# Performance work log

Measured on AMD Instinct MI355X. Metric: run time of the kernel, lower is better.

## Reference

```python
import jax, jax.numpy as jnp
import numpy as np

N_INTT = 100000
N_MVTX = 100000
N_EDGES = 300000
IN_DIM = 64
OUT_DIM = 64
FEAT_DIM = 2 * OUT_DIM          # 128
EDGE_DIM = 2 * FEAT_DIM         # 256
H_DIM = IN_DIM + FEAT_DIM + 2 * EDGE_DIM  # 64+128+512 = 704


def _lin(key, fan_in, fan_out):
    k1, k2 = jax.random.split(key)
    bound = 1.0 / np.sqrt(fan_in)
    W = jax.random.uniform(k1, (fan_in, fan_out), jnp.float32, -bound, bound)
    b = jax.random.uniform(k2, (fan_out,), jnp.float32, -bound, bound)
    return W, b


def setup_inputs() -> dict:
    key = jax.random.key(0)
    ks = jax.random.split(key, 12)
    x_intt_0 = jax.random.normal(ks[0], (N_INTT, 3), jnp.float32)
    x_mvtx_0 = jax.random.normal(ks[1], (N_MVTX, 3), jnp.float32)
    x_intt = jax.random.normal(ks[2], (N_INTT, IN_DIM), jnp.float32)
    x_mvtx = jax.random.normal(ks[3], (N_MVTX, IN_DIM), jnp.float32)
    start = jax.random.randint(ks[4], (N_EDGES,), 0, N_INTT, jnp.int32)
    end = jax.random.randint(ks[5], (N_EDGES,), 0, N_MVTX, jnp.int32)
    edge_index = jnp.stack([start, end], axis=0)
    W_in_intt, b_in_intt = _lin(ks[6], IN_DIM, FEAT_DIM)
    W_in_mvtx, b_in_mvtx = _lin(ks[7], IN_DIM, FEAT_DIM)
    W_score, b_score = _lin(ks[8], EDGE_DIM, 1)
    W_out_intt, b_out_intt = _lin(ks[9], H_DIM, OUT_DIM)
    W_out_mvtx, b_out_mvtx = _lin(ks[10], H_DIM, OUT_DIM)
    return {
        "x_intt_0": x_intt_0, "x_mvtx_0": x_mvtx_0,
        "x_intt": x_intt, "x_mvtx": x_mvtx, "edge_index": edge_index,
        "W_in_intt": W_in_intt, "b_in_intt": b_in_intt,
        "W_in_mvtx": W_in_mvtx, "b_in_mvtx": b_in_mvtx,
        "W_score": W_score, "b_score": b_score,
        "W_out_intt": W_out_intt, "b_out_intt": b_out_intt,
        "W_out_mvtx": W_out_mvtx, "b_out_mvtx": b_out_mvtx,
    }


def _mean_max_pool(edges, idx, num_segments):
    # scatter_mean with zero-initialized out: mean over incident edges, 0 if none
    s = jax.ops.segment_sum(edges, idx, num_segments=num_segments)
    cnt = jax.ops.segment_sum(jnp.ones((edges.shape[0], 1), edges.dtype), idx,
                              num_segments=num_segments)
    mean = s / jnp.maximum(cnt, 1.0)
    # scatter_max with zero-initialized out: max includes the initial 0
    mx = jnp.maximum(jax.ops.segment_max(edges, idx, num_segments=num_segments), 0.0)
    return mean, mx


def reference(x_intt_0, x_mvtx_0, x_intt, x_mvtx, edge_index,
              W_in_intt, b_in_intt, W_in_mvtx, b_in_mvtx,
              W_score, b_score, W_out_intt, b_out_intt,
              W_out_mvtx, b_out_mvtx):
    # apply_constraints=False -> x_intt_0/x_mvtx_0 unused
    xp_intt = x_intt @ W_in_intt + b_in_intt        # [Ni, F]
    xp_mvtx = x_mvtx @ W_in_mvtx + b_in_mvtx        # [Nm, F]
    start, end = edge_index[0], edge_index[1]
    xp = jnp.concatenate([xp_intt[start], xp_mvtx[end]], axis=-1)  # [E, 2F]
    att = jnp.exp(-jnp.abs(xp @ W_score + b_score))  # potential activation, [E,1]
    edges = xp * att                                 # [E, 2F]
    mean_i, max_i = _mean_max_pool(edges, start, xp_intt.shape[0])
    mean_m, max_m = _mean_max_pool(edges, end, xp_mvtx.shape[0])
    H_intt = jnp.concatenate([x_intt, xp_intt, mean_i, max_i], axis=-1)  # [Ni, 704]
    H_mvtx = jnp.concatenate([x_mvtx, xp_mvtx, mean_m, max_m], axis=-1)
    h_intt = jax.nn.relu(H_intt @ W_out_intt + b_out_intt)
    h_mvtx = jax.nn.relu(H_mvtx @ W_out_mvtx + b_out_mvtx)
    return (h_intt, h_mvtx)
```

## Files before the change

kernel.cpp:

```cpp
#include <hip/hip_runtime.h>
#include <hip/hip_bf16.h>

typedef __hip_bfloat16 bf16;
typedef __attribute__((ext_vector_type(8))) short bf16x8;
typedef __attribute__((ext_vector_type(4))) float f32x4;

__device__ __forceinline__ float bfu(unsigned u) { return __uint_as_float(u << 16); }
__device__ __forceinline__ unsigned packbf(float a, float b) {
    return (unsigned)__bfloat16_as_ushort(__float2bfloat16(a)) |
           ((unsigned)__bfloat16_as_ushort(__float2bfloat16(b)) << 16);
}

#define CAP 32

#define NEL_O (704 * 64)

__global__ __launch_bounds__(256) void prep_kernel(
    const int* __restrict__ e_start, const int* __restrict__ e_end,
    int* __restrict__ deg_i, int* __restrict__ deg_m,
    int* __restrict__ list_i, int* __restrict__ list_m, int E, int fill_blocks,
    const float* __restrict__ Woi, const float* __restrict__ Wom,
    bf16* __restrict__ Wtoi, bf16* __restrict__ Wtom,
    const float* __restrict__ Wii, const float* __restrict__ Wim, int wt_blocks,
    const float* __restrict__ x_i, const float* __restrict__ b_i,
    const float* __restrict__ x_m, const float* __restrict__ b_m,
    const float* __restrict__ Wsc,
    bf16* __restrict__ xp_i, bf16* __restrict__ xp_m,
    float* __restrict__ sc_i, float* __restrict__ sc_m,
    int Ni, int Nm, int lin_bi)
{
    int bid = blockIdx.x;
    if (bid < fill_blocks) {
        int i = bid * 256 + threadIdx.x;
        if (i >= E) return;
        int s = e_start[i], e = e_end[i];
        int pi = atomicAdd(&deg_i[s], 1);
        if (pi < CAP) list_i[(size_t)s * CAP + pi] = e;
        int pm = atomicAdd(&deg_m[e], 1);
        if (pm < CAP) list_m[(size_t)e * CAP + pm] = s;
        return;
    }
    bid -= fill_blocks;
    if (bid < wt_blocks) {
        int tid = bid * 256 + threadIdx.x;
        if (tid >= 2 * NEL_O) return;
        int half = tid >= NEL_O;
        int t = tid - half * NEL_O;
        int j = t / 704, k = t % 704;
        const float* W = half ? Wom : Woi;
        bf16* Wt = half ? Wtom : Wtoi;
        Wt[(size_t)j * 704 + k] = __float2bfloat16(W[(size_t)k * 64 + j]);
        return;
    }
    bid -= wt_blocks;
    int side = bid >= lin_bi;
    int blk = side ? bid - lin_bi : bid;
    const float* x   = side ? x_m : x_i;
    const float* Win = side ? Wim : Wii;
    const float* b   = side ? b_m : b_i;
    const float* wsc = side ? Wsc + 128 : Wsc;
    bf16* xp = side ? xp_m : xp_i;
    float* sc = side ? sc_m : sc_i;
    int N = side ? Nm : Ni;

    int tid = threadIdx.x, wv = tid >> 6, lane = tid & 63;
    int frow = lane & 15, kg = lane >> 4;
    int n0 = blk * 64 + wv * 16;
    if (n0 >= N) return;
    int nrow = min(n0 + frow, N - 1);
    f32x4 acc[8];
#pragma unroll
    for (int nt = 0; nt < 8; ++nt) acc[nt] = (f32x4){0.f, 0.f, 0.f, 0.f};
#pragma unroll
    for (int kk = 0; kk < 2; ++kk) {
        const float* ap = x + (size_t)nrow * 64 + kk * 32 + kg * 8;
        float4 a0 = *(const float4*)ap;
        float4 a1 = *(const float4*)(ap + 4);
        union { unsigned u[4]; bf16x8 v; } au;
        au.u[0] = packbf(a0.x, a0.y); au.u[1] = packbf(a0.z, a0.w);
        au.u[2] = packbf(a1.x, a1.y); au.u[3] = packbf(a1.z, a1.w);
#pragma unroll
        for (int nt = 0; nt < 8; ++nt) {
            int col = nt * 16 + frow;
            const float* wp = Win + (size_t)(kk * 32 + kg * 8) * 128 + col;
            union { unsigned u[4]; bf16x8 v; } bu;
#pragma unroll
            for (int z = 0; z < 4; ++z)
                bu.u[z] = packbf(wp[(2 * z) * 128], wp[(2 * z + 1) * 128]);
            acc[nt] = __builtin_amdgcn_mfma_f32_16x16x32_bf16(au.v, bu.v, acc[nt], 0, 0, 0);
        }
    }
    float contrib[4] = {0.f, 0.f, 0.f, 0.f};
#pragma unroll
    for (int nt = 0; nt < 8; ++nt) {
        int col = nt * 16 + frow;
        float bj = b[col];
        float wj = wsc[col];
#pragma unroll
        for (int reg = 0; reg < 4; ++reg) {
            float v = acc[nt][reg] + bj;
            int n = n0 + kg * 4 + reg;
            if (n < N) xp[(size_t)n * 128 + col] = __float2bfloat16(v);
            contrib[reg] += v * wj;
        }
    }
#pragma unroll
    for (int off = 1; off < 16; off <<= 1) {
#pragma unroll
        for (int reg = 0; reg < 4; ++reg)
            contrib[reg] += __shfl_xor(contrib[reg], off, 64);
    }
    if (frow == 0) {
#pragma unroll
        for (int reg = 0; reg < 4; ++reg) {
            int n = n0 + kg * 4 + reg;
            if (n < N) sc[n] = contrib[reg];
        }
    }
}

#define BN 16
#define HS 716
__device__ __forceinline__ void accum8(uint4 g, float att, float* s, float* m) {
    unsigned gg[4] = {g.x, g.y, g.z, g.w};
#pragma unroll
    for (int k = 0; k < 4; ++k) {
        float t0 = att * bfu(gg[k] & 0xffffu);
        float t1 = att * bfu(gg[k] >> 16);
        s[2 * k] += t0;  s[2 * k + 1] += t1;
        m[2 * k] = fmaxf(m[2 * k], t0);  m[2 * k + 1] = fmaxf(m[2 * k + 1], t1);
    }
}

__global__ __launch_bounds__(256) void node_kernel(
    const float* __restrict__ x_i, const bf16* __restrict__ xp_i,
    const bf16* __restrict__ xp_m,
    const float* __restrict__ sc_i, const float* __restrict__ sc_m,
    const int* __restrict__ deg_i, const int* __restrict__ list_i,
    const bf16* __restrict__ Wt_oi, const float* __restrict__ b_oi,
    const float* __restrict__ x_m,
    const int* __restrict__ deg_m, const int* __restrict__ list_m,
    const bf16* __restrict__ Wt_om, const float* __restrict__ b_om,
    const float* __restrict__ bsc, float* __restrict__ out,
    int Ni, int Nm, int blocks_i)
{
    __shared__ bf16 Hs[BN][HS];
    int side = (int)blockIdx.x >= blocks_i;
    int blk = side ? blockIdx.x - blocks_i : blockIdx.x;
    const float* x        = side ? x_m : x_i;
    const bf16* xp_self   = side ? xp_m : xp_i;
    const bf16* xp_other  = side ? xp_i : xp_m;
    const float* sc_self  = side ? sc_m : sc_i;
    const float* sc_other = side ? sc_i : sc_m;
    const int* deg  = side ? deg_m : deg_i;
    const int* list = side ? list_m : list_i;
    const bf16* Wt  = side ? Wt_om : Wt_oi;
    const float* b  = side ? b_om : b_oi;
    float* outp = side ? out + (size_t)Ni * 64 : out;
    int N = side ? Nm : Ni;
    int self_first = side ? 0 : 1;

    int tid = threadIdx.x, wv = tid >> 6, lane = tid & 63;
    int ql = lane & 15, q4 = lane & 48;
    int r = wv * 4 + (lane >> 4);
    int n0 = blk * BN;
    int n = min(n0 + r, N - 1);

    float bias = bsc[0];
    int dg = deg[n];
    int dgc = min(dg, CAP);
    float ps = sc_self[n] + bias;
    uint4 us4 = *(const uint4*)(xp_self + (size_t)n * 128 + ql * 8);
    float4 xv4 = *(const float4*)(x + (size_t)n * 64 + ql * 4);

    int oa = 0, ob = 0;
    float sa = 0.f, sb = 0.f;
    if (ql < dgc)      oa = list[(size_t)n * CAP + ql];
    if (16 + ql < dgc) ob = list[(size_t)n * CAP + 16 + ql];
    if (ql < dgc)      sa = sc_other[oa];
    if (16 + ql < dgc) sb = sc_other[ob];
    float att_a = (ql < dgc)      ? __expf(-fabsf(ps + sa)) : 0.f;
    float att_b = (16 + ql < dgc) ? __expf(-fabsf(ps + sb)) : 0.f;

    float A = att_a + att_b;
    float Am = fmaxf(att_a, att_b);
#pragma unroll
    for (int off = 1; off < 16; off <<= 1) {
        A += __shfl_xor(A, off, 64);
        Am = fmaxf(Am, __shfl_xor(Am, off, 64));
    }

    float s[8], m[8];
#pragma unroll
    for (int k = 0; k < 8; ++k) { s[k] = 0.f; m[k] = 0.f; }

    int dmaxw = dgc;
    dmaxw = max(dmaxw, __shfl_xor(dmaxw, 16, 64));
    dmaxw = max(dmaxw, __shfl_xor(dmaxw, 32, 64));

    int dm0 = min(dmaxw, 16);
    for (int d = 0; d < dm0; d += 4) {
        uint4 g[4];
        float a[4];
#pragma unroll
        for (int j = 0; j < 4; ++j) {
            int dd = min(d + j, 15);
            bool p = (d + j < dgc);
            int o = __shfl(oa, q4 + dd, 64);
            a[j] = p ? __shfl(att_a, q4 + dd, 64) : 0.f;
            g[j] = (uint4){0u, 0u, 0u, 0u};
            if (p) g[j] = *(const uint4*)(xp_other + (size_t)o * 128 + ql * 8);
        }
#pragma unroll
        for (int j = 0; j < 4; ++j) accum8(g[j], a[j], s, m);
    }
    for (int d = 16; d < dmaxw; d += 2) {
#pragma unroll
        for (int j = 0; j < 2; ++j) {
            int dd = min(d + j - 16, 15);
            bool p = (d + j < dgc);
            int o = __shfl(ob, q4 + dd, 64);
            float a0 = p ? __shfl(att_b, q4 + dd, 64) : 0.f;
            uint4 g0 = (uint4){0u, 0u, 0u, 0u};
            if (p) g0 = *(const uint4*)(xp_other + (size_t)o * 128 + ql * 8);
            accum8(g0, a0, s, m);
        }
    }

    float inv = 1.0f / fmaxf((float)dg, 1.0f);
    float sA = A * inv, sAm = Am;
    int cm_self  = self_first ? 192 : 320;
    int cm_cross = self_first ? 320 : 192;
    int cx_self  = self_first ? 448 : 576;
    int cx_cross = self_first ? 576 : 448;
    char* row = (char*)&Hs[r][0];
    *(uint2*)(row + ql * 8) = make_uint2(packbf(xv4.x, xv4.y), packbf(xv4.z, xv4.w));
    *(uint4*)(row + 128 + ql * 16) = us4;
    unsigned uu[4] = {us4.x, us4.y, us4.z, us4.w};
    float xs[8];
#pragma unroll
    for (int k = 0; k < 4; ++k) {
        xs[2 * k] = bfu(uu[k] & 0xffffu);
        xs[2 * k + 1] = bfu(uu[k] >> 16);
    }
    uint4 wms, wxs, wmc, wxc;
    wms.x = packbf(xs[0] * sA, xs[1] * sA);  wms.y = packbf(xs[2] * sA, xs[3] * sA);
    wms.z = packbf(xs[4] * sA, xs[5] * sA);  wms.w = packbf(xs[6] * sA, xs[7] * sA);
    wxs.x = packbf(fmaxf(xs[0], 0.f) * sAm, fmaxf(xs[1], 0.f) * sAm);
    wxs.y = packbf(fmaxf(xs[2], 0.f) * sAm, fmaxf(xs[3], 0.f) * sAm);
    wxs.z = packbf(fmaxf(xs[4], 0.f) * sAm, fmaxf(xs[5], 0.f) * sAm);
    wxs.w = packbf(fmaxf(xs[6], 0.f) * sAm, fmaxf(xs[7], 0.f) * sAm);
    wmc.x = packbf(s[0] * inv, s[1] * inv);  wmc.y = packbf(s[2] * inv, s[3] * inv);
    wmc.z = packbf(s[4] * inv, s[5] * inv);  wmc.w = packbf(s[6] * inv, s[7] * inv);
    wxc.x = packbf(m[0], m[1]);  wxc.y = packbf(m[2], m[3]);
    wxc.z = packbf(m[4], m[5]);  wxc.w = packbf(m[6], m[7]);
    *(uint4*)(row + cm_self * 2 + ql * 16)  = wms;
    *(uint4*)(row + cx_self * 2 + ql * 16)  = wxs;
    *(uint4*)(row + cm_cross * 2 + ql * 16) = wmc;
    *(uint4*)(row + cx_cross * 2 + ql * 16) = wxc;
    __syncthreads();

    int frow = lane & 15;
    int kg = lane >> 4;
    const char* abase = (const char*)&Hs[frow][0] + kg * 16;
    const char* bbase = (const char*)(Wt + (size_t)(wv * 16 + frow) * 704) + kg * 16;
    f32x4 acc = {0.f, 0.f, 0.f, 0.f};
#pragma unroll
    for (int kt = 0; kt < 22; ++kt) {
        bf16x8 a  = *(const bf16x8*)(abase + kt * 64);
        bf16x8 bf = *(const bf16x8*)(bbase + kt * 64);
        acc = __builtin_amdgcn_mfma_f32_16x16x32_bf16(a, bf, acc, 0, 0, 0);
    }
    int ccol = wv * 16 + frow;
    float bj = b[ccol];
#pragma unroll
    for (int reg = 0; reg < 4; ++reg) {
        int crow = kg * 4 + reg;
        int nn = n0 + crow;
        if (nn < N) outp[(size_t)nn * 64 + ccol] = fmaxf(acc[reg] + bj, 0.f);
    }
}

extern "C" void kernel_launch(void* const* d_in, const int* in_sizes, int n_in,
                              void* d_out, int out_size, void* d_ws, size_t ws_size,
                              hipStream_t stream) {
    const float* x_i    = (const float*)d_in[2];
    const float* x_m    = (const float*)d_in[3];
    const int*   eidx   = (const int*)d_in[4];
    const float* W_in_i = (const float*)d_in[5];
    const float* b_in_i = (const float*)d_in[6];
    const float* W_in_m = (const float*)d_in[7];
    const float* b_in_m = (const float*)d_in[8];
    const float* W_sc   = (const float*)d_in[9];
    const float* b_sc   = (const float*)d_in[10];
    const float* W_o_i  = (const float*)d_in[11];
    const float* b_o_i  = (const float*)d_in[12];
    const float* W_o_m  = (const float*)d_in[13];
    const float* b_o_m  = (const float*)d_in[14];

    int Ni = in_sizes[2] / 64;
    int Nm = in_sizes[3] / 64;
    int E  = in_sizes[4] / 2;
    const int* e_start = eidx;
    const int* e_end   = eidx + E;

    char* base = (char*)d_ws;
    bf16* xp_i  = (bf16*)base;  base += (size_t)Ni * 128 * sizeof(bf16);
    bf16* xp_m  = (bf16*)base;  base += (size_t)Nm * 128 * sizeof(bf16);
    float* sc_i = (float*)base; base += (size_t)Ni * sizeof(float);
    float* sc_m = (float*)base; base += (size_t)Nm * sizeof(float);
    int* list_i = (int*)base;   base += (size_t)Ni * CAP * sizeof(int);
    int* list_m = (int*)base;   base += (size_t)Nm * CAP * sizeof(int);
    int* deg_i  = (int*)base;   base += (size_t)Ni * sizeof(int);
    int* deg_m  = (int*)base;   base += (size_t)Nm * sizeof(int);
    bf16* Wt_oi = (bf16*)base;  base += (size_t)704 * 64 * sizeof(bf16);
    bf16* Wt_om = (bf16*)base;  base += (size_t)704 * 64 * sizeof(bf16);
    hipMemsetAsync(deg_i, 0, ((size_t)Ni + Nm) * sizeof(int), stream);

    int fill_blocks = (E + 255) / 256;
    int wt_blocks = (2 * NEL_O + 255) / 256;
    int lin_bi = (Ni + 63) / 64, lin_bm = (Nm + 63) / 64;
    prep_kernel<<<fill_blocks + wt_blocks + lin_bi + lin_bm, 256, 0, stream>>>(
        e_start, e_end, deg_i, deg_m, list_i, list_m, E, fill_blocks,
        W_o_i, W_o_m, Wt_oi, Wt_om, W_in_i, W_in_m, wt_blocks,
        x_i, b_in_i, x_m, b_in_m, W_sc,
        xp_i, xp_m, sc_i, sc_m, Ni, Nm, lin_bi);

    float* out = (float*)d_out;
    int nb_i = (Ni + BN - 1) / BN, nb_m = (Nm + BN - 1) / BN;
    node_kernel<<<nb_i + nb_m, 256, 0, stream>>>(
        x_i, xp_i, xp_m, sc_i, sc_m, deg_i, list_i, Wt_oi, b_o_i,
        x_m, deg_m, list_m, Wt_om, b_o_m, b_sc, out, Ni, Nm, nb_i);
}
```

Before: 221.7 us.

## Assign one wavefront per node in node kernel gather with 1024-thread blocks

Node aggregation now gives each node a full 64-lane wavefront that gathers 4-byte slices of each neighbor row, instead of 16 lanes per node gathering 16-byte slices. Blocks grow to 1024 threads (16 waves, one per node), and only the first four waves run the MFMA output projection. The aim is more memory-level parallelism and more uniform per-wave loop trip counts. In exchange, loads become narrower, there are more shuffles per edge, and 12 of 16 waves sit idle during the matmul phase. The large blocks with launch bounds of (1024, 8) may also limit occupancy or register allocation.

```diff
diff --git a/kernel.cpp b/kernel.cpp
--- a/kernel.cpp
+++ b/kernel.cpp
@@ -121,18 +121,7 @@
 
 #define BN 16
 #define HS 716
-__device__ __forceinline__ void accum8(uint4 g, float att, float* s, float* m) {
-    unsigned gg[4] = {g.x, g.y, g.z, g.w};
-#pragma unroll
-    for (int k = 0; k < 4; ++k) {
-        float t0 = att * bfu(gg[k] & 0xffffu);
-        float t1 = att * bfu(gg[k] >> 16);
-        s[2 * k] += t0;  s[2 * k + 1] += t1;
-        m[2 * k] = fmaxf(m[2 * k], t0);  m[2 * k + 1] = fmaxf(m[2 * k + 1], t1);
-    }
-}
-
-__global__ __launch_bounds__(256) void node_kernel(
+__global__ __launch_bounds__(1024, 8) void node_kernel(
     const float* __restrict__ x_i, const bf16* __restrict__ xp_i,
     const bf16* __restrict__ xp_m,
     const float* __restrict__ sc_i, const float* __restrict__ sc_m,
@@ -161,69 +150,46 @@
     int self_first = side ? 0 : 1;
 
     int tid = threadIdx.x, wv = tid >> 6, lane = tid & 63;
-    int ql = lane & 15, q4 = lane & 48;
-    int r = wv * 4 + (lane >> 4);
     int n0 = blk * BN;
-    int n = min(n0 + r, N - 1);
+    int n = min(n0 + wv, N - 1);
 
     float bias = bsc[0];
     int dg = deg[n];
     int dgc = min(dg, CAP);
     float ps = sc_self[n] + bias;
-    uint4 us4 = *(const uint4*)(xp_self + (size_t)n * 128 + ql * 8);
-    float4 xv4 = *(const float4*)(x + (size_t)n * 64 + ql * 4);
-
-    int oa = 0, ob = 0;
-    float sa = 0.f, sb = 0.f;
-    if (ql < dgc)      oa = list[(size_t)n * CAP + ql];
-    if (16 + ql < dgc) ob = list[(size_t)n * CAP + 16 + ql];
-    if (ql < dgc)      sa = sc_other[oa];
-    if (16 + ql < dgc) sb = sc_other[ob];
-    float att_a = (ql < dgc)      ? __expf(-fabsf(ps + sa)) : 0.f;
-    float att_b = (16 + ql < dgc) ? __expf(-fabsf(ps + sb)) : 0.f;
-
-    float A = att_a + att_b;
-    float Am = fmaxf(att_a, att_b);
-#pragma unroll
-    for (int off = 1; off < 16; off <<= 1) {
+    unsigned us = *(const unsigned*)(xp_self + (size_t)n * 128 + 2 * lane);
+    float xv = x[(size_t)n * 64 + lane];
+
+    int o = (lane < 32) ? list[(size_t)n * CAP + lane] : 0;
+    float sco = (lane < dgc) ? sc_other[o] : 0.f;
+    float att = (lane < dgc) ? __expf(-fabsf(ps + sco)) : 0.f;
+
+    float A = att, Am = att;
+#pragma unroll
+    for (int off = 1; off < 64; off <<= 1) {
         A += __shfl_xor(A, off, 64);
         Am = fmaxf(Am, __shfl_xor(Am, off, 64));
     }
 
-    float s[8], m[8];
-#pragma unroll
-    for (int k = 0; k < 8; ++k) { s[k] = 0.f; m[k] = 0.f; }
-
-    int dmaxw = dgc;
-    dmaxw = max(dmaxw, __shfl_xor(dmaxw, 16, 64));
-    dmaxw = max(dmaxw, __shfl_xor(dmaxw, 32, 64));
-
-    int dm0 = min(dmaxw, 16);
-    for (int d = 0; d < dm0; d += 4) {
-        uint4 g[4];
+    float s0 = 0.f, s1 = 0.f, m0 = 0.f, m1 = 0.f;
+    for (int d = 0; d < dgc; d += 4) {
+        unsigned g[4];
         float a[4];
 #pragma unroll
         for (int j = 0; j < 4; ++j) {
-            int dd = min(d + j, 15);
+            int dd = min(d + j, CAP - 1);
             bool p = (d + j < dgc);
-            int o = __shfl(oa, q4 + dd, 64);
-            a[j] = p ? __shfl(att_a, q4 + dd, 64) : 0.f;
-            g[j] = (uint4){0u, 0u, 0u, 0u};
-            if (p) g[j] = *(const uint4*)(xp_other + (size_t)o * 128 + ql * 8);
-        }
-#pragma unroll
-        for (int j = 0; j < 4; ++j) accum8(g[j], a[j], s, m);
-    }
-    for (int d = 16; d < dmaxw; d += 2) {
-#pragma unroll
-        for (int j = 0; j < 2; ++j) {
-            int dd = min(d + j - 16, 15);
-            bool p = (d + j < dgc);
-            int o = __shfl(ob, q4 + dd, 64);
-            float a0 = p ? __shfl(att_b, q4 + dd, 64) : 0.f;
-            uint4 g0 = (uint4){0u, 0u, 0u, 0u};
-            if (p) g0 = *(const uint4*)(xp_other + (size_t)o * 128 + ql * 8);
-            accum8(g0, a0, s, m);
+            int oo = __shfl(o, dd, 64);
+            a[j] = p ? __shfl(att, dd, 64) : 0.f;
+            g[j] = 0u;
+            if (p) g[j] = *(const unsigned*)(xp_other + (size_t)oo * 128 + 2 * lane);
+        }
+#pragma unroll
+        for (int j = 0; j < 4; ++j) {
+            float t0 = a[j] * bfu(g[j] & 0xffffu);
+            float t1 = a[j] * bfu(g[j] >> 16);
+            s0 += t0;  s1 += t1;
+            m0 = fmaxf(m0, t0);  m1 = fmaxf(m1, t1);
         }
     }
 
@@ -233,33 +199,18 @@
     int cm_cross = self_first ? 320 : 192;
     int cx_self  = self_first ? 448 : 576;
     int cx_cross = self_first ? 576 : 448;
-    char* row = (char*)&Hs[r][0];
-    *(uint2*)(row + ql * 8) = make_uint2(packbf(xv4.x, xv4.y), packbf(xv4.z, xv4.w));
-    *(uint4*)(row + 128 + ql * 16) = us4;
-    unsigned uu[4] = {us4.x, us4.y, us4.z, us4.w};
-    float xs[8];
-#pragma unroll
-    for (int k = 0; k < 4; ++k) {
-        xs[2 * k] = bfu(uu[k] & 0xffffu);
-        xs[2 * k + 1] = bfu(uu[k] >> 16);
-    }
-    uint4 wms, wxs, wmc, wxc;
-    wms.x = packbf(xs[0] * sA, xs[1] * sA);  wms.y = packbf(xs[2] * sA, xs[3] * sA);
-    wms.z = packbf(xs[4] * sA, xs[5] * sA);  wms.w = packbf(xs[6] * sA, xs[7] * sA);
-    wxs.x = packbf(fmaxf(xs[0], 0.f) * sAm, fmaxf(xs[1], 0.f) * sAm);
-    wxs.y = packbf(fmaxf(xs[2], 0.f) * sAm, fmaxf(xs[3], 0.f) * sAm);
-    wxs.z = packbf(fmaxf(xs[4], 0.f) * sAm, fmaxf(xs[5], 0.f) * sAm);
-    wxs.w = packbf(fmaxf(xs[6], 0.f) * sAm, fmaxf(xs[7], 0.f) * sAm);
-    wmc.x = packbf(s[0] * inv, s[1] * inv);  wmc.y = packbf(s[2] * inv, s[3] * inv);
-    wmc.z = packbf(s[4] * inv, s[5] * inv);  wmc.w = packbf(s[6] * inv, s[7] * inv);
-    wxc.x = packbf(m[0], m[1]);  wxc.y = packbf(m[2], m[3]);
-    wxc.z = packbf(m[4], m[5]);  wxc.w = packbf(m[6], m[7]);
-    *(uint4*)(row + cm_self * 2 + ql * 16)  = wms;
-    *(uint4*)(row + cx_self * 2 + ql * 16)  = wxs;
-    *(uint4*)(row + cm_cross * 2 + ql * 16) = wmc;
-    *(uint4*)(row + cx_cross * 2 + ql * 16) = wxc;
+    float xs0 = bfu(us & 0xffffu), xs1 = bfu(us >> 16);
+    char* row = (char*)&Hs[wv][0];
+    ((bf16*)row)[lane] = __float2bfloat16(xv);
+    *(unsigned*)(row + (64 + 2 * lane) * 2)       = us;
+    *(unsigned*)(row + (cm_self + 2 * lane) * 2)  = packbf(xs0 * sA, xs1 * sA);
+    *(unsigned*)(row + (cx_self + 2 * lane) * 2)  = packbf(fmaxf(xs0, 0.f) * sAm,
+                                                           fmaxf(xs1, 0.f) * sAm);
+    *(unsigned*)(row + (cm_cross + 2 * lane) * 2) = packbf(s0 * inv, s1 * inv);
+    *(unsigned*)(row + (cx_cross + 2 * lane) * 2) = packbf(m0, m1);
     __syncthreads();
 
+    if (wv >= 4) return;
     int frow = lane & 15;
     int kg = lane >> 4;
     const char* abase = (const char*)&Hs[frow][0] + kg * 16;
@@ -328,7 +279,7 @@
 
     float* out = (float*)d_out;
     int nb_i = (Ni + BN - 1) / BN, nb_m = (Nm + BN - 1) / BN;
-    node_kernel<<<nb_i + nb_m, 256, 0, stream>>>(
+    node_kernel<<<nb_i + nb_m, 1024, 0, stream>>>(
         x_i, xp_i, xp_m, sc_i, sc_m, deg_i, list_i, Wt_oi, b_o_i,
         x_m, deg_m, list_m, Wt_om, b_o_m, b_sc, out, Ni, Nm, nb_i);
 }
```

New measurement: 286.8 us. +29.4%, slower.

## Replace fixed-capacity adjacency lists with CSR built by count-scan-fill

Applied to the files above, without the earlier changes.

Builds a compact CSR adjacency via degree counting, a block prefix scan and an atomic fill pass, instead of per-node fixed 32-slot lists. Nodes with more than 32 incident edges are now handled through an extra loop. The input features are also cached as bf16 during the projection, and the output store and feature load use nontemporal hints. This reduces adjacency memory footprint and scattered writes, at the cost of two extra kernel launches and a second atomic pass over edges.

```diff
diff --git a/kernel.cpp b/kernel.cpp
--- a/kernel.cpp
+++ b/kernel.cpp
@@ -4,6 +4,7 @@
 typedef __hip_bfloat16 bf16;
 typedef __attribute__((ext_vector_type(8))) short bf16x8;
 typedef __attribute__((ext_vector_type(4))) float f32x4;
+typedef __attribute__((ext_vector_type(2))) unsigned u32x2;
 
 __device__ __forceinline__ float bfu(unsigned u) { return __uint_as_float(u << 16); }
 __device__ __forceinline__ unsigned packbf(float a, float b) {
@@ -11,14 +12,11 @@
            ((unsigned)__bfloat16_as_ushort(__float2bfloat16(b)) << 16);
 }
 
-#define CAP 32
-
 #define NEL_O (704 * 64)
 
 __global__ __launch_bounds__(256) void prep_kernel(
     const int* __restrict__ e_start, const int* __restrict__ e_end,
-    int* __restrict__ deg_i, int* __restrict__ deg_m,
-    int* __restrict__ list_i, int* __restrict__ list_m, int E, int fill_blocks,
+    int* __restrict__ deg_all, int E, int Ni_off, int count_blocks,
     const float* __restrict__ Woi, const float* __restrict__ Wom,
     bf16* __restrict__ Wtoi, bf16* __restrict__ Wtom,
     const float* __restrict__ Wii, const float* __restrict__ Wim, int wt_blocks,
@@ -26,21 +24,19 @@
     const float* __restrict__ x_m, const float* __restrict__ b_m,
     const float* __restrict__ Wsc,
     bf16* __restrict__ xp_i, bf16* __restrict__ xp_m,
+    bf16* __restrict__ xb_i, bf16* __restrict__ xb_m,
     float* __restrict__ sc_i, float* __restrict__ sc_m,
     int Ni, int Nm, int lin_bi)
 {
     int bid = blockIdx.x;
-    if (bid < fill_blocks) {
+    if (bid < count_blocks) {
         int i = bid * 256 + threadIdx.x;
         if (i >= E) return;
-        int s = e_start[i], e = e_end[i];
-        int pi = atomicAdd(&deg_i[s], 1);
-        if (pi < CAP) list_i[(size_t)s * CAP + pi] = e;
-        int pm = atomicAdd(&deg_m[e], 1);
-        if (pm < CAP) list_m[(size_t)e * CAP + pm] = s;
+        atomicAdd(&deg_all[e_start[i]], 1);
+        atomicAdd(&deg_all[Ni_off + e_end[i]], 1);
         return;
     }
-    bid -= fill_blocks;
+    bid -= count_blocks;
     if (bid < wt_blocks) {
         int tid = bid * 256 + threadIdx.x;
         if (tid >= 2 * NEL_O) return;
@@ -60,6 +56,7 @@
     const float* b   = side ? b_m : b_i;
     const float* wsc = side ? Wsc + 128 : Wsc;
     bf16* xp = side ? xp_m : xp_i;
+    bf16* xb = side ? xb_m : xb_i;
     float* sc = side ? sc_m : sc_i;
     int N = side ? Nm : Ni;
 
@@ -79,6 +76,7 @@
         union { unsigned u[4]; bf16x8 v; } au;
         au.u[0] = packbf(a0.x, a0.y); au.u[1] = packbf(a0.z, a0.w);
         au.u[2] = packbf(a1.x, a1.y); au.u[3] = packbf(a1.z, a1.w);
+        *(bf16x8*)(xb + (size_t)nrow * 64 + kk * 32 + kg * 8) = au.v;
 #pragma unroll
         for (int nt = 0; nt < 8; ++nt) {
             int col = nt * 16 + frow;
@@ -119,6 +117,41 @@
     }
 }
 
+__global__ __launch_bounds__(1024) void scan_kernel(
+    const int* __restrict__ deg, int* __restrict__ off, int* __restrict__ cur,
+    int* __restrict__ gcount, int NT)
+{
+    __shared__ int sh[1024];
+    __shared__ int base;
+    int i = blockIdx.x * 1024 + threadIdx.x;
+    int v = (i < NT) ? deg[i] : 0;
+    sh[threadIdx.x] = v;
+    __syncthreads();
+    for (int ofs = 1; ofs < 1024; ofs <<= 1) {
+        int t = (threadIdx.x >= ofs) ? sh[threadIdx.x - ofs] : 0;
+        __syncthreads();
+        sh[threadIdx.x] += t;
+        __syncthreads();
+    }
+    if (threadIdx.x == 1023) base = atomicAdd(gcount, sh[1023]);
+    __syncthreads();
+    int excl = base + sh[threadIdx.x] - v;
+    if (i < NT) { off[i] = excl; cur[i] = excl; }
+}
+
+__global__ __launch_bounds__(256) void fill_kernel(
+    const int* __restrict__ e_start, const int* __restrict__ e_end,
+    int* __restrict__ cur, int* __restrict__ csr, int E, int Ni_off)
+{
+    int i = blockIdx.x * 256 + threadIdx.x;
+    if (i >= E) return;
+    int s = e_start[i], e = e_end[i];
+    int p0 = atomicAdd(&cur[s], 1);
+    csr[p0] = e;
+    int p1 = atomicAdd(&cur[Ni_off + e], 1);
+    csr[p1] = s;
+}
+
 #define BN 16
 #define HS 716
 __device__ __forceinline__ void accum8(uint4 g, float att, float* s, float* m) {
@@ -133,13 +166,13 @@
 }
 
 __global__ __launch_bounds__(256) void node_kernel(
-    const float* __restrict__ x_i, const bf16* __restrict__ xp_i,
+    const bf16* __restrict__ xb_i, const bf16* __restrict__ xp_i,
     const bf16* __restrict__ xp_m,
     const float* __restrict__ sc_i, const float* __restrict__ sc_m,
-    const int* __restrict__ deg_i, const int* __restrict__ list_i,
+    const int* __restrict__ deg_all, const int* __restrict__ off_all,
+    const int* __restrict__ csr,
     const bf16* __restrict__ Wt_oi, const float* __restrict__ b_oi,
-    const float* __restrict__ x_m,
-    const int* __restrict__ deg_m, const int* __restrict__ list_m,
+    const bf16* __restrict__ xb_m,
     const bf16* __restrict__ Wt_om, const float* __restrict__ b_om,
     const float* __restrict__ bsc, float* __restrict__ out,
     int Ni, int Nm, int blocks_i)
@@ -147,17 +180,16 @@
     __shared__ bf16 Hs[BN][HS];
     int side = (int)blockIdx.x >= blocks_i;
     int blk = side ? blockIdx.x - blocks_i : blockIdx.x;
-    const float* x        = side ? x_m : x_i;
+    const bf16* xb        = side ? xb_m : xb_i;
     const bf16* xp_self   = side ? xp_m : xp_i;
     const bf16* xp_other  = side ? xp_i : xp_m;
     const float* sc_self  = side ? sc_m : sc_i;
     const float* sc_other = side ? sc_i : sc_m;
-    const int* deg  = side ? deg_m : deg_i;
-    const int* list = side ? list_m : list_i;
     const bf16* Wt  = side ? Wt_om : Wt_oi;
     const float* b  = side ? b_om : b_oi;
     float* outp = side ? out + (size_t)Ni * 64 : out;
     int N = side ? Nm : Ni;
+    int nid_off = side ? Ni : 0;
     int self_first = side ? 0 : 1;
 
     int tid = threadIdx.x, wv = tid >> 6, lane = tid & 63;
@@ -165,36 +197,38 @@
     int r = wv * 4 + (lane >> 4);
     int n0 = blk * BN;
     int n = min(n0 + r, N - 1);
+    int nid = nid_off + n;
 
     float bias = bsc[0];
-    int dg = deg[n];
-    int dgc = min(dg, CAP);
+    int dg = deg_all[nid];
+    int off = off_all[nid];
     float ps = sc_self[n] + bias;
     uint4 us4 = *(const uint4*)(xp_self + (size_t)n * 128 + ql * 8);
-    float4 xv4 = *(const float4*)(x + (size_t)n * 64 + ql * 4);
-
+    u32x2 xv = __builtin_nontemporal_load((const u32x2*)(xb + (size_t)n * 64 + ql * 4));
+
+    int d16 = min(dg, 16), d32 = min(dg, 32);
     int oa = 0, ob = 0;
     float sa = 0.f, sb = 0.f;
-    if (ql < dgc)      oa = list[(size_t)n * CAP + ql];
-    if (16 + ql < dgc) ob = list[(size_t)n * CAP + 16 + ql];
-    if (ql < dgc)      sa = sc_other[oa];
-    if (16 + ql < dgc) sb = sc_other[ob];
-    float att_a = (ql < dgc)      ? __expf(-fabsf(ps + sa)) : 0.f;
-    float att_b = (16 + ql < dgc) ? __expf(-fabsf(ps + sb)) : 0.f;
+    if (ql < d16)      oa = csr[off + ql];
+    if (16 + ql < d32) ob = csr[off + 16 + ql];
+    if (ql < d16)      sa = sc_other[oa];
+    if (16 + ql < d32) sb = sc_other[ob];
+    float att_a = (ql < d16)      ? __expf(-fabsf(ps + sa)) : 0.f;
+    float att_b = (16 + ql < d32) ? __expf(-fabsf(ps + sb)) : 0.f;
 
     float A = att_a + att_b;
     float Am = fmaxf(att_a, att_b);
 #pragma unroll
-    for (int off = 1; off < 16; off <<= 1) {
-        A += __shfl_xor(A, off, 64);
-        Am = fmaxf(Am, __shfl_xor(Am, off, 64));
+    for (int off2 = 1; off2 < 16; off2 <<= 1) {
+        A += __shfl_xor(A, off2, 64);
+        Am = fmaxf(Am, __shfl_xor(Am, off2, 64));
     }
 
     float s[8], m[8];
 #pragma unroll
     for (int k = 0; k < 8; ++k) { s[k] = 0.f; m[k] = 0.f; }
 
-    int dmaxw = dgc;
+    int dmaxw = dg;
     dmaxw = max(dmaxw, __shfl_xor(dmaxw, 16, 64));
     dmaxw = max(dmaxw, __shfl_xor(dmaxw, 32, 64));
 
@@ -205,7 +239,7 @@
 #pragma unroll
         for (int j = 0; j < 4; ++j) {
             int dd = min(d + j, 15);
-            bool p = (d + j < dgc);
+            bool p = (d + j < dg);
             int o = __shfl(oa, q4 + dd, 64);
             a[j] = p ? __shfl(att_a, q4 + dd, 64) : 0.f;
             g[j] = (uint4){0u, 0u, 0u, 0u};
@@ -214,17 +248,26 @@
 #pragma unroll
         for (int j = 0; j < 4; ++j) accum8(g[j], a[j], s, m);
     }
-    for (int d = 16; d < dmaxw; d += 2) {
+    for (int d = 16; d < min(dmaxw, 32); d += 2) {
 #pragma unroll
         for (int j = 0; j < 2; ++j) {
             int dd = min(d + j - 16, 15);
-            bool p = (d + j < dgc);
+            bool p = (d + j < dg);
             int o = __shfl(ob, q4 + dd, 64);
             float a0 = p ? __shfl(att_b, q4 + dd, 64) : 0.f;
             uint4 g0 = (uint4){0u, 0u, 0u, 0u};
             if (p) g0 = *(const uint4*)(xp_other + (size_t)o * 128 + ql * 8);
             accum8(g0, a0, s, m);
         }
+    }
+    for (int d = 32; d < dmaxw; ++d) {
+        bool p = (d < dg);
+        int o = p ? csr[off + d] : 0;
+        float at = p ? __expf(-fabsf(ps + sc_other[o])) : 0.f;
+        A += at;  Am = fmaxf(Am, at);
+        uint4 g0 = (uint4){0u, 0u, 0u, 0u};
+        if (p) g0 = *(const uint4*)(xp_other + (size_t)o * 128 + ql * 8);
+        accum8(g0, at, s, m);
     }
 
     float inv = 1.0f / fmaxf((float)dg, 1.0f);
@@ -234,7 +277,7 @@
     int cx_self  = self_first ? 448 : 576;
     int cx_cross = self_first ? 576 : 448;
     char* row = (char*)&Hs[r][0];
-    *(uint2*)(row + ql * 8) = make_uint2(packbf(xv4.x, xv4.y), packbf(xv4.z, xv4.w));
+    *(uint2*)(row + ql * 8) = make_uint2(xv.x, xv.y);
     *(uint4*)(row + 128 + ql * 16) = us4;
     unsigned uu[4] = {us4.x, us4.y, us4.z, us4.w};
     float xs[8];
@@ -277,7 +320,9 @@
     for (int reg = 0; reg < 4; ++reg) {
         int crow = kg * 4 + reg;
         int nn = n0 + crow;
-        if (nn < N) outp[(size_t)nn * 64 + ccol] = fmaxf(acc[reg] + bj, 0.f);
+        if (nn < N)
+            __builtin_nontemporal_store(fmaxf(acc[reg] + bj, 0.f),
+                                        &outp[(size_t)nn * 64 + ccol]);
     }
 }
 
@@ -303,32 +348,39 @@
     int E  = in_sizes[4] / 2;
     const int* e_start = eidx;
     const int* e_end   = eidx + E;
+    int NT = Ni + Nm;
 
     char* base = (char*)d_ws;
     bf16* xp_i  = (bf16*)base;  base += (size_t)Ni * 128 * sizeof(bf16);
     bf16* xp_m  = (bf16*)base;  base += (size_t)Nm * 128 * sizeof(bf16);
+    bf16* xb_i  = (bf16*)base;  base += (size_t)Ni * 64 * sizeof(bf16);
+    bf16* xb_m  = (bf16*)base;  base += (size_t)Nm * 64 * sizeof(bf16);
     float* sc_i = (float*)base; base += (size_t)Ni * sizeof(float);
     float* sc_m = (float*)base; base += (size_t)Nm * sizeof(float);
-    int* list_i = (int*)base;   base += (size_t)Ni * CAP * sizeof(int);
-    int* list_m = (int*)base;   base += (size_t)Nm * CAP * sizeof(int);
-    int* deg_i  = (int*)base;   base += (size_t)Ni * sizeof(int);
-    int* deg_m  = (int*)base;   base += (size_t)Nm * sizeof(int);
+    int* off    = (int*)base;   base += (size_t)NT * sizeof(int);
+    int* cur    = (int*)base;   base += (size_t)NT * sizeof(int);
+    int* csr    = (int*)base;   base += (size_t)2 * E * sizeof(int);
     bf16* Wt_oi = (bf16*)base;  base += (size_t)704 * 64 * sizeof(bf16);
     bf16* Wt_om = (bf16*)base;  base += (size_t)704 * 64 * sizeof(bf16);
-    hipMemsetAsync(deg_i, 0, ((size_t)Ni + Nm) * sizeof(int), stream);
-
-    int fill_blocks = (E + 255) / 256;
+    int* deg    = (int*)base;   base += (size_t)NT * sizeof(int);
+    int* gcount = (int*)base;   base += sizeof(int);
+    hipMemsetAsync(deg, 0, ((size_t)NT + 1) * sizeof(int), stream);
+
+    int count_blocks = (E + 255) / 256;
     int wt_blocks = (2 * NEL_O + 255) / 256;
     int lin_bi = (Ni + 63) / 64, lin_bm = (Nm + 63) / 64;
-    prep_kernel<<<fill_blocks + wt_blocks + lin_bi + lin_bm, 256, 0, stream>>>(
-        e_start, e_end, deg_i, deg_m, list_i, list_m, E, fill_blocks,
+    prep_kernel<<<count_blocks + wt_blocks + lin_bi + lin_bm, 256, 0, stream>>>(
+        e_start, e_end, deg, E, Ni, count_blocks,
         W_o_i, W_o_m, Wt_oi, Wt_om, W_in_i, W_in_m, wt_blocks,
         x_i, b_in_i, x_m, b_in_m, W_sc,
-        xp_i, xp_m, sc_i, sc_m, Ni, Nm, lin_bi);
+        xp_i, xp_m, xb_i, xb_m, sc_i, sc_m, Ni, Nm, lin_bi);
+
+    scan_kernel<<<(NT + 1023) / 1024, 1024, 0, stream>>>(deg, off, cur, gcount, NT);
+    fill_kernel<<<(E + 255) / 256, 256, 0, stream>>>(e_start, e_end, cur, csr, E, Ni);
 
     float* out = (float*)d_out;
     int nb_i = (Ni + BN - 1) / BN, nb_m = (Nm + BN - 1) / BN;
     node_kernel<<<nb_i + nb_m, 256, 0, stream>>>(
-        x_i, xp_i, xp_m, sc_i, sc_m, deg_i, list_i, Wt_oi, b_o_i,
-        x_m, deg_m, list_m, Wt_om, b_o_m, b_sc, out, Ni, Nm, nb_i);
-}
+        xb_i, xp_i, xp_m, sc_i, sc_m, deg, off, csr, Wt_oi, b_o_i,
+        xb_m, Wt_om, b_o_m, b_sc, out, Ni, Nm, nb_i);
+}
```

Result: slower. 250.9 us (+13.1%).

## Process 32 nodes per block, reuse weight fragments across two MFMA tiles, cache bf16 x

Applied to the files above, without the earlier changes.

The node kernel now handles 32 nodes per 512-thread block. The output GEMM uses only four waves, each loading a weight fragment once and issuing two MFMAs over two 16-row tiles, so weight traffic per node is halved. The prep kernel also writes a bf16 copy of x that the node kernel reads instead of fp32 x, and output stores are nontemporal. In exchange, half the waves sit idle during the GEMM phase, LDS use per block doubles, and prep does an extra write pass.

```diff
diff --git a/kernel.cpp b/kernel.cpp
--- a/kernel.cpp
+++ b/kernel.cpp
@@ -4,6 +4,7 @@
 typedef __hip_bfloat16 bf16;
 typedef __attribute__((ext_vector_type(8))) short bf16x8;
 typedef __attribute__((ext_vector_type(4))) float f32x4;
+typedef __attribute__((ext_vector_type(2))) unsigned u32x2;
 
 __device__ __forceinline__ float bfu(unsigned u) { return __uint_as_float(u << 16); }
 __device__ __forceinline__ unsigned packbf(float a, float b) {
@@ -12,7 +13,6 @@
 }
 
 #define CAP 32
-
 #define NEL_O (704 * 64)
 
 __global__ __launch_bounds__(256) void prep_kernel(
@@ -26,6 +26,7 @@
     const float* __restrict__ x_m, const float* __restrict__ b_m,
     const float* __restrict__ Wsc,
     bf16* __restrict__ xp_i, bf16* __restrict__ xp_m,
+    bf16* __restrict__ xb_i, bf16* __restrict__ xb_m,
     float* __restrict__ sc_i, float* __restrict__ sc_m,
     int Ni, int Nm, int lin_bi)
 {
@@ -60,6 +61,7 @@
     const float* b   = side ? b_m : b_i;
     const float* wsc = side ? Wsc + 128 : Wsc;
     bf16* xp = side ? xp_m : xp_i;
+    bf16* xb = side ? xb_m : xb_i;
     float* sc = side ? sc_m : sc_i;
     int N = side ? Nm : Ni;
 
@@ -79,6 +81,7 @@
         union { unsigned u[4]; bf16x8 v; } au;
         au.u[0] = packbf(a0.x, a0.y); au.u[1] = packbf(a0.z, a0.w);
         au.u[2] = packbf(a1.x, a1.y); au.u[3] = packbf(a1.z, a1.w);
+        *(bf16x8*)(xb + (size_t)nrow * 64 + kk * 32 + kg * 8) = au.v;
 #pragma unroll
         for (int nt = 0; nt < 8; ++nt) {
             int col = nt * 16 + frow;
@@ -119,7 +122,7 @@
     }
 }
 
-#define BN 16
+#define BN 32
 #define HS 716
 __device__ __forceinline__ void accum8(uint4 g, float att, float* s, float* m) {
     unsigned gg[4] = {g.x, g.y, g.z, g.w};
@@ -132,13 +135,13 @@
     }
 }
 
-__global__ __launch_bounds__(256) void node_kernel(
-    const float* __restrict__ x_i, const bf16* __restrict__ xp_i,
+__global__ __launch_bounds__(512, 6) void node_kernel(
+    const bf16* __restrict__ xb_i, const bf16* __restrict__ xp_i,
     const bf16* __restrict__ xp_m,
     const float* __restrict__ sc_i, const float* __restrict__ sc_m,
     const int* __restrict__ deg_i, const int* __restrict__ list_i,
     const bf16* __restrict__ Wt_oi, const float* __restrict__ b_oi,
-    const float* __restrict__ x_m,
+    const bf16* __restrict__ xb_m,
     const int* __restrict__ deg_m, const int* __restrict__ list_m,
     const bf16* __restrict__ Wt_om, const float* __restrict__ b_om,
     const float* __restrict__ bsc, float* __restrict__ out,
@@ -147,7 +150,7 @@
     __shared__ bf16 Hs[BN][HS];
     int side = (int)blockIdx.x >= blocks_i;
     int blk = side ? blockIdx.x - blocks_i : blockIdx.x;
-    const float* x        = side ? x_m : x_i;
+    const bf16* xb        = side ? xb_m : xb_i;
     const bf16* xp_self   = side ? xp_m : xp_i;
     const bf16* xp_other  = side ? xp_i : xp_m;
     const float* sc_self  = side ? sc_m : sc_i;
@@ -171,15 +174,16 @@
     int dgc = min(dg, CAP);
     float ps = sc_self[n] + bias;
     uint4 us4 = *(const uint4*)(xp_self + (size_t)n * 128 + ql * 8);
-    float4 xv4 = *(const float4*)(x + (size_t)n * 64 + ql * 4);
-
+    u32x2 xv = __builtin_nontemporal_load((const u32x2*)(xb + (size_t)n * 64 + ql * 4));
+
+    int d16 = min(dgc, 16);
     int oa = 0, ob = 0;
     float sa = 0.f, sb = 0.f;
-    if (ql < dgc)      oa = list[(size_t)n * CAP + ql];
+    if (ql < d16)      oa = list[(size_t)n * CAP + ql];
     if (16 + ql < dgc) ob = list[(size_t)n * CAP + 16 + ql];
-    if (ql < dgc)      sa = sc_other[oa];
+    if (ql < d16)      sa = sc_other[oa];
     if (16 + ql < dgc) sb = sc_other[ob];
-    float att_a = (ql < dgc)      ? __expf(-fabsf(ps + sa)) : 0.f;
+    float att_a = (ql < d16)      ? __expf(-fabsf(ps + sa)) : 0.f;
     float att_b = (16 + ql < dgc) ? __expf(-fabsf(ps + sb)) : 0.f;
 
     float A = att_a + att_b;
@@ -234,7 +238,7 @@
     int cx_self  = self_first ? 448 : 576;
     int cx_cross = self_first ? 576 : 448;
     char* row = (char*)&Hs[r][0];
-    *(uint2*)(row + ql * 8) = make_uint2(packbf(xv4.x, xv4.y), packbf(xv4.z, xv4.w));
+    *(uint2*)(row + ql * 8) = make_uint2(xv.x, xv.y);
     *(uint4*)(row + 128 + ql * 16) = us4;
     unsigned uu[4] = {us4.x, us4.y, us4.z, us4.w};
     float xs[8];
@@ -260,24 +264,35 @@
     *(uint4*)(row + cx_cross * 2 + ql * 16) = wxc;
     __syncthreads();
 
+    if (wv >= 4) return;
     int frow = lane & 15;
     int kg = lane >> 4;
-    const char* abase = (const char*)&Hs[frow][0] + kg * 16;
+    const char* abase0 = (const char*)&Hs[frow][0] + kg * 16;
+    const char* abase1 = (const char*)&Hs[16 + frow][0] + kg * 16;
     const char* bbase = (const char*)(Wt + (size_t)(wv * 16 + frow) * 704) + kg * 16;
-    f32x4 acc = {0.f, 0.f, 0.f, 0.f};
+    f32x4 acc0 = {0.f, 0.f, 0.f, 0.f};
+    f32x4 acc1 = {0.f, 0.f, 0.f, 0.f};
 #pragma unroll
     for (int kt = 0; kt < 22; ++kt) {
-        bf16x8 a  = *(const bf16x8*)(abase + kt * 64);
         bf16x8 bf = *(const bf16x8*)(bbase + kt * 64);
-        acc = __builtin_amdgcn_mfma_f32_16x16x32_bf16(a, bf, acc, 0, 0, 0);
+        bf16x8 a0 = *(const bf16x8*)(abase0 + kt * 64);
+        bf16x8 a1 = *(const bf16x8*)(abase1 + kt * 64);
+        acc0 = __builtin_amdgcn_mfma_f32_16x16x32_bf16(a0, bf, acc0, 0, 0, 0);
+        acc1 = __builtin_amdgcn_mfma_f32_16x16x32_bf16(a1, bf, acc1, 0, 0, 0);
     }
     int ccol = wv * 16 + frow;
     float bj = b[ccol];
 #pragma unroll
     for (int reg = 0; reg < 4; ++reg) {
         int crow = kg * 4 + reg;
-        int nn = n0 + crow;
-        if (nn < N) outp[(size_t)nn * 64 + ccol] = fmaxf(acc[reg] + bj, 0.f);
+        int nn0 = n0 + crow;
+        int nn1 = n0 + 16 + crow;
+        if (nn0 < N)
+            __builtin_nontemporal_store(fmaxf(acc0[reg] + bj, 0.f),
+                                        &outp[(size_t)nn0 * 64 + ccol]);
+        if (nn1 < N)
+            __builtin_nontemporal_store(fmaxf(acc1[reg] + bj, 0.f),
+                                        &outp[(size_t)nn1 * 64 + ccol]);
     }
 }
 
@@ -307,14 +322,16 @@
     char* base = (char*)d_ws;
     bf16* xp_i  = (bf16*)base;  base += (size_t)Ni * 128 * sizeof(bf16);
     bf16* xp_m  = (bf16*)base;  base += (size_t)Nm * 128 * sizeof(bf16);
+    bf16* xb_i  = (bf16*)base;  base += (size_t)Ni * 64 * sizeof(bf16);
+    bf16* xb_m  = (bf16*)base;  base += (size_t)Nm * 64 * sizeof(bf16);
     float* sc_i = (float*)base; base += (size_t)Ni * sizeof(float);
     float* sc_m = (float*)base; base += (size_t)Nm * sizeof(float);
     int* list_i = (int*)base;   base += (size_t)Ni * CAP * sizeof(int);
     int* list_m = (int*)base;   base += (size_t)Nm * CAP * sizeof(int);
+    bf16* Wt_oi = (bf16*)base;  base += (size_t)704 * 64 * sizeof(bf16);
+    bf16* Wt_om = (bf16*)base;  base += (size_t)704 * 64 * sizeof(bf16);
     int* deg_i  = (int*)base;   base += (size_t)Ni * sizeof(int);
     int* deg_m  = (int*)base;   base += (size_t)Nm * sizeof(int);
-    bf16* Wt_oi = (bf16*)base;  base += (size_t)704 * 64 * sizeof(bf16);
-    bf16* Wt_om = (bf16*)base;  base += (size_t)704 * 64 * sizeof(bf16);
     hipMemsetAsync(deg_i, 0, ((size_t)Ni + Nm) * sizeof(int), stream);
 
     int fill_blocks = (E + 255) / 256;
@@ -324,11 +341,11 @@
         e_start, e_end, deg_i, deg_m, list_i, list_m, E, fill_blocks,
         W_o_i, W_o_m, Wt_oi, Wt_om, W_in_i, W_in_m, wt_blocks,
         x_i, b_in_i, x_m, b_in_m, W_sc,
-        xp_i, xp_m, sc_i, sc_m, Ni, Nm, lin_bi);
+        xp_i, xp_m, xb_i, xb_m, sc_i, sc_m, Ni, Nm, lin_bi);
 
     float* out = (float*)d_out;
     int nb_i = (Ni + BN - 1) / BN, nb_m = (Nm + BN - 1) / BN;
-    node_kernel<<<nb_i + nb_m, 256, 0, stream>>>(
-        x_i, xp_i, xp_m, sc_i, sc_m, deg_i, list_i, Wt_oi, b_o_i,
-        x_m, deg_m, list_m, Wt_om, b_o_m, b_sc, out, Ni, Nm, nb_i);
-}
+    node_kernel<<<nb_i + nb_m, 512, 0, stream>>>(
+        xb_i, xp_i, xp_m, sc_i, sc_m, deg_i, list_i, Wt_oi, b_o_i,
+        xb_m, deg_m, list_m, Wt_om, b_o_m, b_sc, out, Ni, Nm, nb_i);
+}
```

Measured after the change: 228.0 us. 2.8% more time.
